# Kernel optimization log

Measured on AMD Instinct MI355X. Metric: run time of the kernel, lower is better.

Reference implementation:

```python
import jax, jax.numpy as jnp
import numpy as np

NUM_HEADS = 8

def setup_inputs() -> dict:
    key = jax.random.key(0)
    k1, k2, k3 = jax.random.split(key, 3)
    B, N, C = 4, 4096, 512
    x = jax.random.normal(k1, (B, N, C), dtype=jnp.float32)
    w_qkv = jax.random.normal(k2, (C, 3 * C), dtype=jnp.float32) * (1.0 / np.sqrt(C))
    w_proj = jax.random.normal(k3, (C, C), dtype=jnp.float32) * (1.0 / np.sqrt(C))
    b_proj = jnp.zeros((C,), dtype=jnp.float32)
    return {"x": x, "w_qkv": w_qkv, "w_proj": w_proj, "b_proj": b_proj}

def reference(x, w_qkv, w_proj, b_proj):
    B, N, C = x.shape
    H = NUM_HEADS
    D = C // H
    # qkv projection (no bias), split into q, k, v of shape [B, H, N, D]
    qkv = (x @ w_qkv).reshape(B, N, 3, H, D)
    qkv = jnp.transpose(qkv, (2, 0, 3, 1, 4))
    q, k, v = qkv[0], qkv[1], qkv[2]
    # q: softmax over head_dim; k: elu(k)+1 then softmax over sequence dim
    q = jax.nn.softmax(q, axis=-1)
    k = jax.nn.softmax(jax.nn.elu(k) + 1.0, axis=-2)
    # linear attention: context = k^T @ v  -> [B, H, D, D]
    context = jnp.einsum('bhnd,bhne->bhde', k, v)
    # out = q @ context -> [B, H, N, D]
    out = jnp.einsum('bhnd,bhde->bhne', q, context)
    out = jnp.transpose(out, (0, 2, 1, 3)).reshape(B, N, C)
    # output projection (dropout with p=0.0 is identity)
    return out @ w_proj + b_proj
```

## Files before the change

### kernel.cpp

```cpp
#include <hip/hip_runtime.h>
#include <hip/hip_bf16.h>

typedef unsigned short u16;
typedef __attribute__((ext_vector_type(8))) short bhalf8;
typedef __attribute__((ext_vector_type(4))) float fx4;

struct __align__(8) US4 { u16 v[4]; };

__device__ __forceinline__ u16 f2bf(float x) {
  union { float f; unsigned int u; } c; c.f = x;
  unsigned int r = c.u + 0x7FFFu + ((c.u >> 16) & 1u);
  return (u16)(r >> 16);
}

__device__ __forceinline__ void gload16(const void* g, void* l) {
  __builtin_amdgcn_global_load_lds((const __attribute__((address_space(1))) void*)g,
                                   (__attribute__((address_space(3))) void*)l,
                                   16, 0, 0);
}

#define MFMA16(a, b, c) __builtin_amdgcn_mfma_f32_16x16x32_bf16((a), (b), (c), 0, 0, 0)
#define FENCE() asm volatile("" ::: "memory")

__global__ void k_conv(const float* __restrict__ in, u16* __restrict__ out, int n4) {
  int i = blockIdx.x * 256 + threadIdx.x;
  if (i < n4) {
    float4 v = ((const float4*)in)[i];
    US4 o;
    o.v[0] = f2bf(v.x); o.v[1] = f2bf(v.y); o.v[2] = f2bf(v.z); o.v[3] = f2bf(v.w);
    ((US4*)out)[i] = o;
  }
}

__global__ void k_transpose(const float* __restrict__ in, u16* __restrict__ out,
                            int R, int C, int rtiles, int remap) {
  __shared__ float tile[64][65];
  const int bx = blockIdx.x;
  const int rt = bx % rtiles, ct = bx / rtiles;
  const int r0 = rt * 64, c0 = ct * 64;
  const int t = threadIdx.x;
  #pragma unroll
  for (int i = 0; i < 16; ++i) {
    int e = i * 256 + t;
    int rr = e >> 6, cc = e & 63;
    tile[rr][cc] = in[(r0 + rr) * C + c0 + cc];
  }
  __syncthreads();
  #pragma unroll
  for (int i = 0; i < 16; ++i) {
    int e = i * 256 + t;
    int rr = e >> 6, cc = e & 63;
    int orow = c0 + rr;
    if (remap && orow >= 512) {
      int region = (orow - 512) >> 9;
      int within = (orow - 512) & 511;
      int h = within >> 6;
      orow = 512 + h * 128 + region * 64 + (within & 63);
    }
    out[orow * R + r0 + cc] = f2bf(tile[cc][rr]);
  }
}

__device__ __forceinline__ void gemm_core2(const char* Ab, const char* Bb,
                                           char* lds, fx4 acc[4][4]) {
  const int t = threadIdx.x;
  const int w = t >> 6, l = t & 63;
  const int wm = w >> 1, wn = w & 1;

  #define STAGE_A(buf, kt, j) do {                                   \
    int off_ = ((j) * 512 + t) * 16;                                 \
    int row_ = off_ >> 7;                                            \
    int scol_ = (off_ & 127) ^ ((row_ & 7) << 4);                    \
    gload16(Ab + row_ * 1024 + (kt) * 128 + scol_,                   \
            lds + (buf) * 49152 + off_);                             \
  } while (0)
  #define STAGE_B(buf, kt, j) do {                                   \
    int off_ = ((j) * 512 + t) * 16;                                 \
    int row_ = off_ >> 7;                                            \
    int scol_ = (off_ & 127) ^ ((row_ & 7) << 4);                    \
    gload16(Bb + row_ * 1024 + (kt) * 128 + scol_,                   \
            lds + (buf) * 49152 + 32768 + off_);                     \
  } while (0)

  #pragma unroll
  for (int j = 0; j < 4; ++j) STAGE_A(0, 0, j);
  #pragma unroll
  for (int j = 0; j < 2; ++j) STAGE_B(0, 0, j);
  #pragma unroll
  for (int j = 0; j < 4; ++j) STAGE_A(1, 1, j);
  #pragma unroll
  for (int j = 0; j < 2; ++j) STAGE_B(1, 1, j);
  asm volatile("s_waitcnt vmcnt(6)" ::: "memory");
  __builtin_amdgcn_s_barrier();
  FENCE();
  __builtin_amdgcn_sched_barrier(0);

  #pragma unroll 1
  for (int kt = 0; kt < 8; ++kt) {
    const int p = kt % 3;
    const char* As = lds + p * 49152;
    const char* Bs = As + 32768;
    const int np = (kt + 2) % 3;
    bhalf8 af[4], bfv[4];
    #pragma unroll
    for (int ks = 0; ks < 2; ++ks) {
      const int kbyte = ks * 64 + ((l >> 4) * 16);
      #pragma unroll
      for (int f = 0; f < 4; ++f) {
        int ra = wm * 64 + f * 16 + (l & 15);
        af[f] = *(const bhalf8*)(As + ra * 128 + (kbyte ^ ((ra & 7) << 4)));
        int rb = wn * 64 + f * 16 + (l & 15);
        bfv[f] = *(const bhalf8*)(Bs + rb * 128 + (kbyte ^ ((rb & 7) << 4)));
      }
      if (kt < 6) {
        if (ks == 0) { STAGE_A(np, kt + 2, 0); STAGE_A(np, kt + 2, 1); STAGE_B(np, kt + 2, 0); }
        else         { STAGE_A(np, kt + 2, 2); STAGE_A(np, kt + 2, 3); STAGE_B(np, kt + 2, 1); }
      }
      __builtin_amdgcn_s_barrier();
      asm volatile("s_waitcnt lgkmcnt(0)" ::: "memory");
      __builtin_amdgcn_sched_barrier(0);
      __builtin_amdgcn_s_setprio(1);
      #pragma unroll
      for (int fm = 0; fm < 4; ++fm)
        #pragma unroll
        for (int fn = 0; fn < 4; ++fn)
          acc[fm][fn] = MFMA16(af[fm], bfv[fn], acc[fm][fn]);
      __builtin_amdgcn_s_setprio(0);
      if (ks == 1) {
        if (kt < 6) asm volatile("s_waitcnt vmcnt(6)" ::: "memory");
        else        asm volatile("s_waitcnt vmcnt(0)" ::: "memory");
      }
      __builtin_amdgcn_s_barrier();
      FENCE();
      __builtin_amdgcn_sched_barrier(0);
    }
  }
  #undef STAGE_A
  #undef STAGE_B
}

__global__ __launch_bounds__(512, 2)
void k_qkv_gemm(const char* __restrict__ xb, const char* __restrict__ wqT,
                u16* __restrict__ qhat, float* __restrict__ ctx_part,
                float* __restrict__ z_part) {
  __shared__ __align__(16) char lds[147456];
  const int bx = blockIdx.x;
  const int tM = bx & 63, tN = bx >> 6;
  fx4 acc[4][4];
  const fx4 z4 = {0.f, 0.f, 0.f, 0.f};
  #pragma unroll
  for (int i = 0; i < 4; ++i)
    #pragma unroll
    for (int j = 0; j < 4; ++j) acc[i][j] = z4;

  gemm_core2(xb + tM * 262144, wqT + tN * 131072, lds, acc);

  const int t = threadIdx.x, w = t >> 6, l = t & 63;
  const int wm = w >> 1, wn = w & 1;
  const int m0 = tM * 256 + wm * 64;
  const int c0 = tN * 128 + wn * 64;

  if (tN < 4) {
    #pragma unroll
    for (int fm = 0; fm < 4; ++fm) {
      #pragma unroll
      for (int fn = 0; fn < 4; ++fn)
        #pragma unroll
        for (int r = 0; r < 4; ++r)
          acc[fm][fn][r] = __expf(acc[fm][fn][r]);
      fx4 s = acc[fm][0] + acc[fm][1] + acc[fm][2] + acc[fm][3];
      fx4 inv;
      #pragma unroll
      for (int r = 0; r < 4; ++r) {
        float sv = s[r];
        sv += __shfl_xor(sv, 1, 64);
        sv += __shfl_xor(sv, 2, 64);
        sv += __shfl_xor(sv, 4, 64);
        sv += __shfl_xor(sv, 8, 64);
        inv[r] = 1.0f / sv;
      }
      #pragma unroll
      for (int fn = 0; fn < 4; ++fn)
        #pragma unroll
        for (int r = 0; r < 4; ++r) {
          int m = m0 + fm * 16 + ((l >> 4) * 4) + r;
          int c = c0 + fn * 16 + (l & 15);
          qhat[m * 512 + c] = f2bf(acc[fm][fn][r] * inv[r]);
        }
    }
  } else {
    const int h = tN - 4;
    const int b = tM >> 4;
    const int mt = tM & 15;
    const int bh = b * 8 + h;
    char* ktb = lds;
    char* vtb = lds + 32768;
    __syncthreads();
    {
      char* dstb = (wn == 0) ? ktb : vtb;
      const bool isK = (wn == 0);
      #pragma unroll
      for (int fm = 0; fm < 4; ++fm)
        #pragma unroll
        for (int fn = 0; fn < 4; ++fn) {
          int d = fn * 16 + (l & 15);
          int n0 = wm * 64 + fm * 16 + ((l >> 4) * 4);
          US4 p;
          #pragma unroll
          for (int r = 0; r < 4; ++r) {
            float v = acc[fm][fn][r];
            if (isK) { float tt = v > 0.f ? v + 1.f : __expf(v); v = __expf(tt); }
            p.v[r] = f2bf(v);
          }
          *(US4*)(dstb + d * 512 + ((2 * n0) ^ ((d & 7) << 4))) = p;
        }
    }
    __syncthreads();
    fx4 cacc[2]; fx4 zacc = z4;
    cacc[0] = z4; cacc[1] = z4;
    bhalf8 ones;
    #pragma unroll
    for (int i = 0; i < 8; ++i) ones[i] = (short)0x3F80;
    #pragma unroll
    for (int kk = 0; kk < 8; ++kk) {
      int nbyte = kk * 64 + ((l >> 4) * 16);
      int d = wm * 16 + (l & 15);
      bhalf8 a = *(const bhalf8*)(ktb + d * 512 + (nbyte ^ ((d & 7) << 4)));
      #pragma unroll
      for (int fn = 0; fn < 2; ++fn) {
        int e = wn * 32 + fn * 16 + (l & 15);
        bhalf8 bv = *(const bhalf8*)(vtb + e * 512 + (nbyte ^ ((e & 7) << 4)));
        cacc[fn] = MFMA16(a, bv, cacc[fn]);
      }
      if (wn == 0) zacc = MFMA16(a, ones, zacc);
    }
    float* cp = ctx_part + (bh * 16 + mt) * 4096;
    #pragma unroll
    for (int fn = 0; fn < 2; ++fn)
      #pragma unroll
      for (int r = 0; r < 4; ++r) {
        int d = wm * 16 + ((l >> 4) * 4) + r;
        int e = wn * 32 + fn * 16 + (l & 15);
        cp[d * 64 + e] = cacc[fn][r];
      }
    if (wn == 0 && (l & 15) == 0) {
      #pragma unroll
      for (int r = 0; r < 4; ++r)
        z_part[(bh * 16 + mt) * 64 + wm * 16 + ((l >> 4) * 4) + r] = zacc[r];
    }
  }
}

__global__ __launch_bounds__(256)
void k_reduce(const float* __restrict__ ctx_part, float* __restrict__ ctx32) {
  const int bx = blockIdx.x;
  const int bh = bx >> 4;
  const int idx = (bx & 15) * 256 + threadIdx.x;
  float s = 0.f;
  #pragma unroll
  for (int mt = 0; mt < 16; ++mt)
    s += ctx_part[(bh * 16 + mt) * 4096 + idx];
  ctx32[bh * 4096 + idx] = s;
}

__global__ __launch_bounds__(256, 1)
void k_w2(const float* __restrict__ ctx32, const float* __restrict__ z_part,
          const u16* __restrict__ wpT, u16* __restrict__ W2T) {
  const int bh = blockIdx.x;
  const int b = bh >> 3, h = bh & 7;
  __shared__ float zinv[64];
  __shared__ __align__(16) u16 alds[64][72];
  const int t = threadIdx.x;
  if (t < 64) {
    float zs = 0.f;
    #pragma unroll
    for (int mt = 0; mt < 16; ++mt) zs += z_part[(bh * 16 + mt) * 64 + t];
    zinv[t] = 1.0f / zs;
  }
  __syncthreads();
  #pragma unroll
  for (int i = 0; i < 16; ++i) {
    int idx = i * 256 + t;
    int d = idx >> 6, e = idx & 63;
    alds[d][e] = f2bf(ctx32[bh * 4096 + idx] * zinv[d]);
  }
  __syncthreads();
  const int w = t >> 6, l = t & 63;
  fx4 acc[4][8];
  const fx4 z4 = {0.f, 0.f, 0.f, 0.f};
  #pragma unroll
  for (int i = 0; i < 4; ++i)
    #pragma unroll
    for (int j = 0; j < 8; ++j) acc[i][j] = z4;
  #pragma unroll
  for (int ks = 0; ks < 2; ++ks) {
    bhalf8 af[4];
    #pragma unroll
    for (int fm = 0; fm < 4; ++fm) {
      int row = fm * 16 + (l & 15);
      af[fm] = *(const bhalf8*)((const char*)alds + row * 144 + ks * 64 + ((l >> 4) * 16));
    }
    #pragma unroll
    for (int fn = 0; fn < 8; ++fn) {
      int c = w * 128 + fn * 16 + (l & 15);
      bhalf8 bv = *(const bhalf8*)(wpT + c * 512 + h * 64 + ks * 32 + ((l >> 4) * 8));
      #pragma unroll
      for (int fm = 0; fm < 4; ++fm)
        acc[fm][fn] = MFMA16(af[fm], bv, acc[fm][fn]);
    }
  }
  #pragma unroll
  for (int fm = 0; fm < 4; ++fm)
    #pragma unroll
    for (int fn = 0; fn < 8; ++fn) {
      int c = w * 128 + fn * 16 + (l & 15);
      int d0 = fm * 16 + ((l >> 4) * 4);
      US4 p;
      #pragma unroll
      for (int r = 0; r < 4; ++r) p.v[r] = f2bf(acc[fm][fn][r]);
      *(US4*)(W2T + (b * 512 + c) * 512 + h * 64 + d0) = p;
    }
}

__global__ __launch_bounds__(512, 2)
void k_out_gemm(const char* __restrict__ qhat, const char* __restrict__ W2T,
                const float* __restrict__ bproj, float* __restrict__ outp) {
  __shared__ __align__(16) char lds[147456];
  const int bx = blockIdx.x;
  const int tM = bx & 63, tN = bx >> 6;
  const int b = tM >> 4;
  fx4 acc[4][4];
  const fx4 z4 = {0.f, 0.f, 0.f, 0.f};
  #pragma unroll
  for (int i = 0; i < 4; ++i)
    #pragma unroll
    for (int j = 0; j < 4; ++j) acc[i][j] = z4;

  gemm_core2(qhat + tM * 262144, W2T + b * 524288 + tN * 131072, lds, acc);

  const int t = threadIdx.x, w = t >> 6, l = t & 63;
  const int wm = w >> 1, wn = w & 1;
  const int m0 = tM * 256 + wm * 64;
  const int c0 = tN * 128 + wn * 64;
  #pragma unroll
  for (int fm = 0; fm < 4; ++fm)
    #pragma unroll
    for (int fn = 0; fn < 4; ++fn) {
      int c = c0 + fn * 16 + (l & 15);
      float bp = bproj[c];
      #pragma unroll
      for (int r = 0; r < 4; ++r) {
        int m = m0 + fm * 16 + ((l >> 4) * 4) + r;
        outp[m * 512 + c] = acc[fm][fn][r] + bp;
      }
    }
}

extern "C" void kernel_launch(void* const* d_in, const int* in_sizes, int n_in,
                              void* d_out, int out_size, void* d_ws, size_t ws_size,
                              hipStream_t stream) {
  (void)in_sizes; (void)n_in; (void)out_size;
  const float* x     = (const float*)d_in[0];
  const float* wqkv  = (const float*)d_in[1];
  const float* wproj = (const float*)d_in[2];
  const float* bproj = (const float*)d_in[3];
  float* outp = (float*)d_out;
  char* ws = (char*)d_ws;

  char* xb   = ws;
  char* wqT  = ws + 16777216;
  char* wpT  = ws + 18350080;
  char* qhat = ws + 18874368;
  char* ctxp = ws + 35651584;
  char* zp   = ws + 44040192;
  char* ctx32= ws + 44171264;
  char* w2t  = ws + 44695552;
  if (ws_size < 46792704) return;

  k_conv<<<8192, 256, 0, stream>>>(x, (u16*)xb, 2097152);
  k_transpose<<<192, 256, 0, stream>>>(wqkv, (u16*)wqT, 512, 1536, 8, 1);
  k_transpose<<<64, 256, 0, stream>>>(wproj, (u16*)wpT, 512, 512, 8, 0);
  k_qkv_gemm<<<768, 512, 0, stream>>>(xb, wqT, (u16*)qhat, (float*)ctxp, (float*)zp);
  k_reduce<<<512, 256, 0, stream>>>((const float*)ctxp, (float*)ctx32);
  k_w2<<<32, 256, 0, stream>>>((const float*)ctx32, (const float*)zp, (const u16*)wpT, (u16*)w2t);
  k_out_gemm<<<256, 512, 0, stream>>>(qhat, w2t, bproj, outp);
}
```

Before: 88.27 us.

## Enlarge GEMM tiles to 256x256 with quadrant-split double-buffered pipeline

After: 95.42 us. 8.1% more time.

```diff
diff --git a/kernel.cpp b/kernel.cpp
--- a/kernel.cpp
+++ b/kernel.cpp
@@ -61,114 +61,183 @@
   }
 }
 
-__device__ __forceinline__ void gemm_core2(const char* Ab, const char* Bb,
-                                           char* lds, fx4 acc[4][4]) {
+__device__ __forceinline__ void gemm_core3(const char* __restrict__ Ab,
+                                           const char* __restrict__ Bb,
+                                           char* lds, fx4 acc[8][4]) {
   const int t = threadIdx.x;
-  const int w = t >> 6, l = t & 63;
-  const int wm = w >> 1, wn = w & 1;
-
-  #define STAGE_A(buf, kt, j) do {                                   \
-    int off_ = ((j) * 512 + t) * 16;                                 \
-    int row_ = off_ >> 7;                                            \
-    int scol_ = (off_ & 127) ^ ((row_ & 7) << 4);                    \
-    gload16(Ab + row_ * 1024 + (kt) * 128 + scol_,                   \
-            lds + (buf) * 49152 + off_);                             \
+  const int l = t & 63;
+  const int w = t >> 6;
+  const int wm = w >> 2, wn = w & 3;
+
+  #define STAGE_AH(buf, kt, hf, j) do {                              \
+    int ra_ = (j) * 64 + (t >> 3);                                   \
+    int col_ = (t & 7) * 16;                                         \
+    int m_ = (ra_ & 63) | ((ra_ >> 6) << 7) | ((hf) << 6);           \
+    gload16(Ab + m_ * 1024 + (kt) * 128 + (col_ ^ ((ra_ & 7) << 4)), \
+            lds + (buf) * 65536 + (hf) * 16384 + (j) * 8192 + t * 16); \
   } while (0)
-  #define STAGE_B(buf, kt, j) do {                                   \
-    int off_ = ((j) * 512 + t) * 16;                                 \
-    int row_ = off_ >> 7;                                            \
-    int scol_ = (off_ & 127) ^ ((row_ & 7) << 4);                    \
-    gload16(Bb + row_ * 1024 + (kt) * 128 + scol_,                   \
-            lds + (buf) * 49152 + 32768 + off_);                     \
+  #define STAGE_BH(buf, kt, hf, j) do {                              \
+    int rb_ = (j) * 64 + (t >> 3);                                   \
+    int col_ = (t & 7) * 16;                                         \
+    int c_ = (rb_ & 31) | ((rb_ >> 5) << 6) | ((hf) << 5);           \
+    gload16(Bb + c_ * 1024 + (kt) * 128 + (col_ ^ ((rb_ & 7) << 4)), \
+            lds + (buf) * 65536 + 32768 + (hf) * 16384 + (j) * 8192 + t * 16); \
   } while (0)
 
-  #pragma unroll
-  for (int j = 0; j < 4; ++j) STAGE_A(0, 0, j);
-  #pragma unroll
-  for (int j = 0; j < 2; ++j) STAGE_B(0, 0, j);
-  #pragma unroll
-  for (int j = 0; j < 4; ++j) STAGE_A(1, 1, j);
-  #pragma unroll
-  for (int j = 0; j < 2; ++j) STAGE_B(1, 1, j);
-  asm volatile("s_waitcnt vmcnt(6)" ::: "memory");
+  STAGE_AH(0, 0, 0, 0); STAGE_AH(0, 0, 0, 1);
+  STAGE_BH(0, 0, 0, 0); STAGE_BH(0, 0, 0, 1);
+  STAGE_BH(0, 0, 1, 0); STAGE_BH(0, 0, 1, 1);
+  STAGE_AH(0, 0, 1, 0); STAGE_AH(0, 0, 1, 1);
+  asm volatile("s_waitcnt vmcnt(4)" ::: "memory");
   __builtin_amdgcn_s_barrier();
   FENCE();
   __builtin_amdgcn_sched_barrier(0);
 
   #pragma unroll 1
   for (int kt = 0; kt < 8; ++kt) {
-    const int p = kt % 3;
-    const char* As = lds + p * 49152;
+    const char* As = lds + (kt & 1) * 65536;
     const char* Bs = As + 32768;
-    const int np = (kt + 2) % 3;
-    bhalf8 af[4], bfv[4];
+    const int nb = (kt + 1) & 1;
+    const bool nt = (kt < 7);
+    bhalf8 a[8], b0[4], b1[4];
+
     #pragma unroll
     for (int ks = 0; ks < 2; ++ks) {
-      const int kbyte = ks * 64 + ((l >> 4) * 16);
-      #pragma unroll
-      for (int f = 0; f < 4; ++f) {
-        int ra = wm * 64 + f * 16 + (l & 15);
-        af[f] = *(const bhalf8*)(As + ra * 128 + (kbyte ^ ((ra & 7) << 4)));
-        int rb = wn * 64 + f * 16 + (l & 15);
-        bfv[f] = *(const bhalf8*)(Bs + rb * 128 + (kbyte ^ ((rb & 7) << 4)));
-      }
-      if (kt < 6) {
-        if (ks == 0) { STAGE_A(np, kt + 2, 0); STAGE_A(np, kt + 2, 1); STAGE_B(np, kt + 2, 0); }
-        else         { STAGE_A(np, kt + 2, 2); STAGE_A(np, kt + 2, 3); STAGE_B(np, kt + 2, 1); }
-      }
-      __builtin_amdgcn_s_barrier();
-      asm volatile("s_waitcnt lgkmcnt(0)" ::: "memory");
-      __builtin_amdgcn_sched_barrier(0);
-      __builtin_amdgcn_s_setprio(1);
+      const int kb = ks * 64 + ((l >> 4) * 16);
+      #pragma unroll
+      for (int fm = 0; fm < 4; ++fm) {
+        int ra = wm * 64 + fm * 16 + (l & 15);
+        a[ks * 4 + fm] = *(const bhalf8*)(As + ra * 128 + (kb ^ ((ra & 7) << 4)));
+      }
+      #pragma unroll
+      for (int fn = 0; fn < 2; ++fn) {
+        int rb = wn * 32 + fn * 16 + (l & 15);
+        b0[ks * 2 + fn] = *(const bhalf8*)(Bs + rb * 128 + (kb ^ ((rb & 7) << 4)));
+      }
+    }
+    if (nt) { STAGE_AH(nb, kt + 1, 0, 0); STAGE_AH(nb, kt + 1, 0, 1); }
+    __builtin_amdgcn_s_barrier();
+    asm volatile("s_waitcnt lgkmcnt(0)" ::: "memory");
+    __builtin_amdgcn_sched_barrier(0);
+    __builtin_amdgcn_s_setprio(1);
+    #pragma unroll
+    for (int ks = 0; ks < 2; ++ks)
       #pragma unroll
       for (int fm = 0; fm < 4; ++fm)
         #pragma unroll
-        for (int fn = 0; fn < 4; ++fn)
-          acc[fm][fn] = MFMA16(af[fm], bfv[fn], acc[fm][fn]);
-      __builtin_amdgcn_s_setprio(0);
-      if (ks == 1) {
-        if (kt < 6) asm volatile("s_waitcnt vmcnt(6)" ::: "memory");
-        else        asm volatile("s_waitcnt vmcnt(0)" ::: "memory");
-      }
-      __builtin_amdgcn_s_barrier();
-      FENCE();
-      __builtin_amdgcn_sched_barrier(0);
-    }
-  }
-  #undef STAGE_A
-  #undef STAGE_B
+        for (int fn = 0; fn < 2; ++fn)
+          acc[fm][fn] = MFMA16(a[ks * 4 + fm], b0[ks * 2 + fn], acc[fm][fn]);
+    __builtin_amdgcn_s_setprio(0);
+    if (nt) asm volatile("s_waitcnt vmcnt(4)" ::: "memory");
+    else    asm volatile("s_waitcnt vmcnt(2)" ::: "memory");
+    __builtin_amdgcn_s_barrier();
+    FENCE();
+    __builtin_amdgcn_sched_barrier(0);
+
+    #pragma unroll
+    for (int ks = 0; ks < 2; ++ks) {
+      const int kb = ks * 64 + ((l >> 4) * 16);
+      #pragma unroll
+      for (int fn = 0; fn < 2; ++fn) {
+        int rb = wn * 32 + fn * 16 + (l & 15);
+        b1[ks * 2 + fn] = *(const bhalf8*)(Bs + 16384 + rb * 128 + (kb ^ ((rb & 7) << 4)));
+      }
+    }
+    if (nt) { STAGE_BH(nb, kt + 1, 0, 0); STAGE_BH(nb, kt + 1, 0, 1); }
+    __builtin_amdgcn_s_barrier();
+    asm volatile("s_waitcnt lgkmcnt(0)" ::: "memory");
+    __builtin_amdgcn_sched_barrier(0);
+    __builtin_amdgcn_s_setprio(1);
+    #pragma unroll
+    for (int ks = 0; ks < 2; ++ks)
+      #pragma unroll
+      for (int fm = 0; fm < 4; ++fm)
+        #pragma unroll
+        for (int fn = 0; fn < 2; ++fn)
+          acc[fm][2 + fn] = MFMA16(a[ks * 4 + fm], b1[ks * 2 + fn], acc[fm][2 + fn]);
+    __builtin_amdgcn_s_setprio(0);
+    if (nt) asm volatile("s_waitcnt vmcnt(4)" ::: "memory");
+    else    asm volatile("s_waitcnt vmcnt(0)" ::: "memory");
+    __builtin_amdgcn_s_barrier();
+    FENCE();
+    __builtin_amdgcn_sched_barrier(0);
+
+    #pragma unroll
+    for (int ks = 0; ks < 2; ++ks) {
+      const int kb = ks * 64 + ((l >> 4) * 16);
+      #pragma unroll
+      for (int fm = 0; fm < 4; ++fm) {
+        int ra = wm * 64 + fm * 16 + (l & 15);
+        a[ks * 4 + fm] = *(const bhalf8*)(As + 16384 + ra * 128 + (kb ^ ((ra & 7) << 4)));
+      }
+    }
+    if (nt) { STAGE_BH(nb, kt + 1, 1, 0); STAGE_BH(nb, kt + 1, 1, 1); }
+    __builtin_amdgcn_s_barrier();
+    asm volatile("s_waitcnt lgkmcnt(0)" ::: "memory");
+    __builtin_amdgcn_sched_barrier(0);
+    __builtin_amdgcn_s_setprio(1);
+    #pragma unroll
+    for (int ks = 0; ks < 2; ++ks)
+      #pragma unroll
+      for (int fm = 0; fm < 4; ++fm)
+        #pragma unroll
+        for (int fn = 0; fn < 2; ++fn)
+          acc[4 + fm][2 + fn] = MFMA16(a[ks * 4 + fm], b1[ks * 2 + fn], acc[4 + fm][2 + fn]);
+    __builtin_amdgcn_s_setprio(0);
+    __builtin_amdgcn_s_barrier();
+    FENCE();
+    __builtin_amdgcn_sched_barrier(0);
+
+    if (nt) { STAGE_AH(nb, kt + 1, 1, 0); STAGE_AH(nb, kt + 1, 1, 1); }
+    __builtin_amdgcn_s_barrier();
+    __builtin_amdgcn_s_setprio(1);
+    #pragma unroll
+    for (int ks = 0; ks < 2; ++ks)
+      #pragma unroll
+      for (int fm = 0; fm < 4; ++fm)
+        #pragma unroll
+        for (int fn = 0; fn < 2; ++fn)
+          acc[4 + fm][fn] = MFMA16(a[ks * 4 + fm], b0[ks * 2 + fn], acc[4 + fm][fn]);
+    __builtin_amdgcn_s_setprio(0);
+    if (nt) asm volatile("s_waitcnt vmcnt(4)" ::: "memory");
+    __builtin_amdgcn_s_barrier();
+    FENCE();
+    __builtin_amdgcn_sched_barrier(0);
+  }
+  #undef STAGE_AH
+  #undef STAGE_BH
 }
 
 __global__ __launch_bounds__(512, 2)
 void k_qkv_gemm(const char* __restrict__ xb, const char* __restrict__ wqT,
                 u16* __restrict__ qhat, float* __restrict__ ctx_part,
                 float* __restrict__ z_part) {
-  __shared__ __align__(16) char lds[147456];
+  __shared__ __align__(16) char lds[131072];
   const int bx = blockIdx.x;
   const int tM = bx & 63, tN = bx >> 6;
-  fx4 acc[4][4];
+  fx4 acc[8][4];
   const fx4 z4 = {0.f, 0.f, 0.f, 0.f};
   #pragma unroll
-  for (int i = 0; i < 4; ++i)
+  for (int i = 0; i < 8; ++i)
     #pragma unroll
     for (int j = 0; j < 4; ++j) acc[i][j] = z4;
 
-  gemm_core2(xb + tM * 262144, wqT + tN * 131072, lds, acc);
+  gemm_core3(xb + tM * 262144, wqT + tN * 262144, lds, acc);
 
   const int t = threadIdx.x, w = t >> 6, l = t & 63;
-  const int wm = w >> 1, wn = w & 1;
-  const int m0 = tM * 256 + wm * 64;
-  const int c0 = tN * 128 + wn * 64;
-
-  if (tN < 4) {
-    #pragma unroll
-    for (int fm = 0; fm < 4; ++fm) {
-      #pragma unroll
-      for (int fn = 0; fn < 4; ++fn)
+  const int wm = w >> 2, wn = w & 3;
+
+  if (tN < 2) {
+    const int m0 = tM * 256 + wm * 128;
+    const int c0 = tN * 256 + wn * 64;
+    #pragma unroll
+    for (int i = 0; i < 8; ++i) {
+      #pragma unroll
+      for (int j = 0; j < 4; ++j)
         #pragma unroll
         for (int r = 0; r < 4; ++r)
-          acc[fm][fn][r] = __expf(acc[fm][fn][r]);
-      fx4 s = acc[fm][0] + acc[fm][1] + acc[fm][2] + acc[fm][3];
+          acc[i][j][r] = __expf(acc[i][j][r]);
+      fx4 s = acc[i][0] + acc[i][1] + acc[i][2] + acc[i][3];
       fx4 inv;
       #pragma unroll
       for (int r = 0; r < 4; ++r) {
@@ -180,73 +249,69 @@
         inv[r] = 1.0f / sv;
       }
       #pragma unroll
-      for (int fn = 0; fn < 4; ++fn)
+      for (int j = 0; j < 4; ++j)
         #pragma unroll
         for (int r = 0; r < 4; ++r) {
-          int m = m0 + fm * 16 + ((l >> 4) * 4) + r;
-          int c = c0 + fn * 16 + (l & 15);
-          qhat[m * 512 + c] = f2bf(acc[fm][fn][r] * inv[r]);
+          int m = m0 + i * 16 + ((l >> 4) * 4) + r;
+          int c = c0 + j * 16 + (l & 15);
+          qhat[m * 512 + c] = f2bf(acc[i][j][r] * inv[r]);
         }
     }
   } else {
-    const int h = tN - 4;
-    const int b = tM >> 4;
-    const int mt = tM & 15;
-    const int bh = b * 8 + h;
-    char* ktb = lds;
-    char* vtb = lds + 32768;
+    const int j2 = tN - 2;
+    const int b = tM >> 4, mt = tM & 15;
+    const int hl = wn >> 1;
+    const bool isK = ((wn & 1) == 0);
+    const int bh = b * 8 + j2 * 2 + hl;
+    char* kbuf = lds + hl * 65536;
+    char* vbuf = kbuf + 32768;
+    char* dstb = isK ? kbuf : vbuf;
+    #pragma unroll
+    for (int i = 0; i < 8; ++i)
+      #pragma unroll
+      for (int j = 0; j < 4; ++j) {
+        int d = j * 16 + (l & 15);
+        int n0 = wm * 128 + i * 16 + ((l >> 4) * 4);
+        US4 p;
+        #pragma unroll
+        for (int r = 0; r < 4; ++r) {
+          float v = acc[i][j][r];
+          if (isK) { float tt = v > 0.f ? v + 1.f : __expf(v); v = __expf(tt); }
+          p.v[r] = f2bf(v);
+        }
+        *(US4*)(dstb + d * 512 + ((2 * n0) ^ ((d & 7) << 4))) = p;
+      }
     __syncthreads();
-    {
-      char* dstb = (wn == 0) ? ktb : vtb;
-      const bool isK = (wn == 0);
-      #pragma unroll
-      for (int fm = 0; fm < 4; ++fm)
-        #pragma unroll
-        for (int fn = 0; fn < 4; ++fn) {
-          int d = fn * 16 + (l & 15);
-          int n0 = wm * 64 + fm * 16 + ((l >> 4) * 4);
-          US4 p;
-          #pragma unroll
-          for (int r = 0; r < 4; ++r) {
-            float v = acc[fm][fn][r];
-            if (isK) { float tt = v > 0.f ? v + 1.f : __expf(v); v = __expf(tt); }
-            p.v[r] = f2bf(v);
-          }
-          *(US4*)(dstb + d * 512 + ((2 * n0) ^ ((d & 7) << 4))) = p;
-        }
-    }
-    __syncthreads();
-    fx4 cacc[2]; fx4 zacc = z4;
-    cacc[0] = z4; cacc[1] = z4;
+    const int d0 = (wm * 2 + (wn & 1)) * 16;
+    fx4 cacc[4]; fx4 zacc = z4;
+    #pragma unroll
+    for (int fe = 0; fe < 4; ++fe) cacc[fe] = z4;
     bhalf8 ones;
     #pragma unroll
     for (int i = 0; i < 8; ++i) ones[i] = (short)0x3F80;
     #pragma unroll
     for (int kk = 0; kk < 8; ++kk) {
-      int nbyte = kk * 64 + ((l >> 4) * 16);
-      int d = wm * 16 + (l & 15);
-      bhalf8 a = *(const bhalf8*)(ktb + d * 512 + (nbyte ^ ((d & 7) << 4)));
-      #pragma unroll
-      for (int fn = 0; fn < 2; ++fn) {
-        int e = wn * 32 + fn * 16 + (l & 15);
-        bhalf8 bv = *(const bhalf8*)(vtb + e * 512 + (nbyte ^ ((e & 7) << 4)));
-        cacc[fn] = MFMA16(a, bv, cacc[fn]);
-      }
-      if (wn == 0) zacc = MFMA16(a, ones, zacc);
+      int kb = kk * 64 + ((l >> 4) * 16);
+      int d = d0 + (l & 15);
+      bhalf8 a = *(const bhalf8*)(kbuf + d * 512 + (kb ^ ((d & 7) << 4)));
+      #pragma unroll
+      for (int fe = 0; fe < 4; ++fe) {
+        int e = fe * 16 + (l & 15);
+        bhalf8 bv = *(const bhalf8*)(vbuf + e * 512 + (kb ^ ((e & 7) << 4)));
+        cacc[fe] = MFMA16(a, bv, cacc[fe]);
+      }
+      zacc = MFMA16(a, ones, zacc);
     }
     float* cp = ctx_part + (bh * 16 + mt) * 4096;
     #pragma unroll
-    for (int fn = 0; fn < 2; ++fn)
-      #pragma unroll
-      for (int r = 0; r < 4; ++r) {
-        int d = wm * 16 + ((l >> 4) * 4) + r;
-        int e = wn * 32 + fn * 16 + (l & 15);
-        cp[d * 64 + e] = cacc[fn][r];
-      }
-    if (wn == 0 && (l & 15) == 0) {
+    for (int fe = 0; fe < 4; ++fe)
       #pragma unroll
       for (int r = 0; r < 4; ++r)
-        z_part[(bh * 16 + mt) * 64 + wm * 16 + ((l >> 4) * 4) + r] = zacc[r];
+        cp[(d0 + (l >> 4) * 4 + r) * 64 + fe * 16 + (l & 15)] = cacc[fe][r];
+    if ((l & 15) == 0) {
+      #pragma unroll
+      for (int r = 0; r < 4; ++r)
+        z_part[(bh * 16 + mt) * 64 + d0 + (l >> 4) * 4 + r] = zacc[r];
     }
   }
 }
@@ -325,33 +390,33 @@
 __global__ __launch_bounds__(512, 2)
 void k_out_gemm(const char* __restrict__ qhat, const char* __restrict__ W2T,
                 const float* __restrict__ bproj, float* __restrict__ outp) {
-  __shared__ __align__(16) char lds[147456];
+  __shared__ __align__(16) char lds[131072];
   const int bx = blockIdx.x;
   const int tM = bx & 63, tN = bx >> 6;
   const int b = tM >> 4;
-  fx4 acc[4][4];
+  fx4 acc[8][4];
   const fx4 z4 = {0.f, 0.f, 0.f, 0.f};
   #pragma unroll
-  for (int i = 0; i < 4; ++i)
+  for (int i = 0; i < 8; ++i)
     #pragma unroll
     for (int j = 0; j < 4; ++j) acc[i][j] = z4;
 
-  gemm_core2(qhat + tM * 262144, W2T + b * 524288 + tN * 131072, lds, acc);
+  gemm_core3(qhat + tM * 262144, W2T + b * 524288 + tN * 262144, lds, acc);
 
   const int t = threadIdx.x, w = t >> 6, l = t & 63;
-  const int wm = w >> 1, wn = w & 1;
-  const int m0 = tM * 256 + wm * 64;
-  const int c0 = tN * 128 + wn * 64;
-  #pragma unroll
-  for (int fm = 0; fm < 4; ++fm)
-    #pragma unroll
-    for (int fn = 0; fn < 4; ++fn) {
-      int c = c0 + fn * 16 + (l & 15);
+  const int wm = w >> 2, wn = w & 3;
+  const int m0 = tM * 256 + wm * 128;
+  const int c0 = tN * 256 + wn * 64;
+  #pragma unroll
+  for (int i = 0; i < 8; ++i)
+    #pragma unroll
+    for (int j = 0; j < 4; ++j) {
+      int c = c0 + j * 16 + (l & 15);
       float bp = bproj[c];
       #pragma unroll
       for (int r = 0; r < 4; ++r) {
-        int m = m0 + fm * 16 + ((l >> 4) * 4) + r;
-        outp[m * 512 + c] = acc[fm][fn][r] + bp;
+        int m = m0 + i * 16 + ((l >> 4) * 4) + r;
+        outp[m * 512 + c] = acc[i][j][r] + bp;
       }
     }
 }
@@ -380,8 +445,8 @@
   k_conv<<<8192, 256, 0, stream>>>(x, (u16*)xb, 2097152);
   k_transpose<<<192, 256, 0, stream>>>(wqkv, (u16*)wqT, 512, 1536, 8, 1);
   k_transpose<<<64, 256, 0, stream>>>(wproj, (u16*)wpT, 512, 512, 8, 0);
-  k_qkv_gemm<<<768, 512, 0, stream>>>(xb, wqT, (u16*)qhat, (float*)ctxp, (float*)zp);
+  k_qkv_gemm<<<384, 512, 0, stream>>>(xb, wqT, (u16*)qhat, (float*)ctxp, (float*)zp);
   k_reduce<<<512, 256, 0, stream>>>((const float*)ctxp, (float*)ctx32);
   k_w2<<<32, 256, 0, stream>>>((const float*)ctx32, (const float*)zp, (const u16*)wpT, (u16*)w2t);
-  k_out_gemm<<<256, 512, 0, stream>>>(qhat, w2t, bproj, outp);
-}
+  k_out_gemm<<<128, 512, 0, stream>>>(qhat, w2t, bproj, outp);
+}
```
